# Performance work log

Hardware: AMD Instinct MI355X
Metric: run time of the kernel (lower is better)

Reference implementation:

```python
import jax, jax.numpy as jnp
import numpy as np

N_NODES = 50000
N_EDGES = 800000
VOCAB = 15000
IN_FEATS = 128
HIDDEN = 32
HEADS = 4
N_GRAPHS = 64
NEG_SLOPE = 0.2


def setup_inputs() -> dict:
    key = jax.random.key(0)
    ks = jax.random.split(key, 16)
    word_ids = jax.random.randint(ks[0], (N_NODES,), 0, VOCAB)
    edge_src = jax.random.randint(ks[1], (N_EDGES,), 0, N_NODES)
    edge_dst = jax.random.randint(ks[2], (N_EDGES,), 0, N_NODES)
    node_graph_id = jnp.sort(jax.random.randint(ks[3], (N_NODES,), 0, N_GRAPHS))
    y_data = jax.random.uniform(ks[4], (N_GRAPHS,))
    word_embeds = jax.random.normal(ks[5], (VOCAB, IN_FEATS)) * 0.02
    W0 = jax.random.normal(ks[6], (IN_FEATS, HEADS * HIDDEN)) * (1.0 / np.sqrt(IN_FEATS))
    al0 = jax.random.normal(ks[7], (HEADS, HIDDEN)) * 0.1
    ar0 = jax.random.normal(ks[8], (HEADS, HIDDEN)) * 0.1
    W1 = jax.random.normal(ks[9], (HEADS * HIDDEN, HEADS * HIDDEN)) * (1.0 / np.sqrt(HEADS * HIDDEN))
    al1 = jax.random.normal(ks[10], (HEADS, HIDDEN)) * 0.1
    ar1 = jax.random.normal(ks[11], (HEADS, HIDDEN)) * 0.1
    out_w = jax.random.normal(ks[12], (HEADS * HIDDEN, 1)) * (1.0 / np.sqrt(HEADS * HIDDEN))
    out_b = jnp.zeros((1,))
    return {"word_ids": word_ids, "edge_src": edge_src, "edge_dst": edge_dst,
            "node_graph_id": node_graph_id, "y_data": y_data,
            "word_embeds": word_embeds, "W0": W0, "al0": al0, "ar0": ar0,
            "W1": W1, "al1": al1, "ar1": ar1, "out_w": out_w, "out_b": out_b}


def gat_layer(h, src, dst, W, al, ar):
    # h: [N, Fin] -> feat: [N, H, D]
    feat = (h @ W).reshape(N_NODES, HEADS, HIDDEN)
    el = (feat * al[None]).sum(-1)  # [N, H]
    er = (feat * ar[None]).sum(-1)  # [N, H]
    e = jax.nn.leaky_relu(el[src] + er[dst], NEG_SLOPE)  # [E, H]
    # segment softmax over incoming edges of each dst node
    m = jax.ops.segment_max(e, dst, num_segments=N_NODES)
    m = jnp.where(jnp.isfinite(m), m, 0.0)
    ex = jnp.exp(e - m[dst])
    denom = jax.ops.segment_sum(ex, dst, num_segments=N_NODES)
    alpha = ex / (denom[dst] + 1e-10)  # [E, H]
    msg = feat[src] * alpha[:, :, None]  # [E, H, D]
    out = jax.ops.segment_sum(msg, dst, num_segments=N_NODES)  # [N, H, D]
    return jax.nn.elu(out).reshape(N_NODES, HEADS * HIDDEN)


def reference(word_ids, edge_src, edge_dst, node_graph_id, y_data,
              word_embeds, W0, al0, ar0, W1, al1, ar1, out_w, out_b):
    h = word_embeds[word_ids]  # [N, IN_FEATS]
    h = gat_layer(h, edge_src, edge_dst, W0, al0, ar0)
    h = gat_layer(h, edge_src, edge_dst, W1, al1, ar1)
    # per-graph max pooling over nodes
    pooled = jax.ops.segment_max(h, node_graph_id, num_segments=N_GRAPHS)
    pooled = jnp.where(jnp.isfinite(pooled), pooled, 0.0)  # guard empty graphs
    logits = (pooled @ out_w + out_b).reshape(-1)  # [G]
    # BCE with logits (stable)
    loss = jnp.mean(jnp.maximum(logits, 0.0) - logits * y_data
                    + jnp.log1p(jnp.exp(-jnp.abs(logits))))
    y_pred = jax.nn.sigmoid(logits)[:, None]
    return (loss, y_pred)
```

## Files before the change

kernel.cpp:

```cpp
#include <hip/hip_runtime.h>
#include <math.h>

#define N_NODES 50000
#define N_EDGES 800000
#define HEADS 4
#define N_GRAPHS 64
#define NEG_SLOPE 0.2f
#define LOG2E 1.4426950408889634f
#define SCAN_NB 196
#define POOL_CHUNK 200
#define POOL_NB 250
#define FEAT_NB 782
#define EDGE_Q 200000
#define EDGE_NB 782

typedef __attribute__((ext_vector_type(8))) short bf16x8;
typedef __attribute__((ext_vector_type(4))) float f32x4;

__device__ __forceinline__ unsigned fkey(float f) {
    unsigned u = __float_as_uint(f);
    return (u & 0x80000000u) ? ~u : (u | 0x80000000u);
}
__device__ __forceinline__ float kval(unsigned k) {
    unsigned u = (k & 0x80000000u) ? (k & 0x7FFFFFFFu) : ~k;
    return __uint_as_float(u);
}

__device__ __forceinline__ unsigned short f2bf(float f) {
    unsigned u = __float_as_uint(f);
    u += 0x7FFFu + ((u >> 16) & 1u);
    return (unsigned short)(u >> 16);
}
__device__ __forceinline__ unsigned pack_bf2(float a, float b) {
    return (unsigned)f2bf(a) | ((unsigned)f2bf(b) << 16);
}


__global__ void hist_kernel(const int* __restrict__ dst, int* __restrict__ deg,
                            int* __restrict__ rank) {
    int i = blockIdx.x * 256 + threadIdx.x;
    if (i >= EDGE_Q) return;
    int e0 = i, e1 = i + EDGE_Q, e2 = i + 2 * EDGE_Q, e3 = i + 3 * EDGE_Q;
    int d0 = dst[e0], d1 = dst[e1], d2 = dst[e2], d3 = dst[e3];
    int r0 = atomicAdd(&deg[d0], 1);
    int r1 = atomicAdd(&deg[d1], 1);
    int r2 = atomicAdd(&deg[d2], 1);
    int r3 = atomicAdd(&deg[d3], 1);
    rank[e0] = r0; rank[e1] = r1; rank[e2] = r2; rank[e3] = r3;
}

__global__ void partial_kernel(const int* __restrict__ deg, int* __restrict__ partial) {
    int t = threadIdx.x, b = blockIdx.x;
    int i = b * 256 + t;
    int v = (i < N_NODES) ? deg[i] : 0;
    #pragma unroll
    for (int off = 1; off < 64; off <<= 1) v += __shfl_xor(v, off, 64);
    __shared__ int wsum[4];
    if ((t & 63) == 0) wsum[t >> 6] = v;
    __syncthreads();
    if (t == 0) partial[b] = wsum[0] + wsum[1] + wsum[2] + wsum[3];
}

__global__ void csr_offsets_kernel(const int* __restrict__ deg, const int* __restrict__ partial,
                                   int* __restrict__ row_start) {
    __shared__ int sb[SCAN_NB];
    __shared__ int wsumA[4];
    __shared__ int wsumB[4];
    int t = threadIdx.x, b = blockIdx.x;
    int lane = t & 63, w = t >> 6;
    {
        int v = (t < SCAN_NB) ? partial[t] : 0;
        int incl = v;
        #pragma unroll
        for (int off = 1; off < 64; off <<= 1) {
            int u = __shfl_up(incl, off, 64);
            if (lane >= off) incl += u;
        }
        if (lane == 63) wsumA[w] = incl;
        __syncthreads();
        int woff = 0;
        #pragma unroll
        for (int k = 0; k < 4; ++k) if (k < w) woff += wsumA[k];
        if (t < SCAN_NB) sb[t] = woff + incl - v;
        __syncthreads();
    }
    int i = b * 256 + t;
    int v = (i < N_NODES) ? deg[i] : 0;
    int incl = v;
    #pragma unroll
    for (int off = 1; off < 64; off <<= 1) {
        int u = __shfl_up(incl, off, 64);
        if (lane >= off) incl += u;
    }
    if (lane == 63) wsumB[w] = incl;
    __syncthreads();
    int woff = sb[b];
    #pragma unroll
    for (int k = 0; k < 4; ++k) if (k < w) woff += wsumB[k];
    int excl = woff + incl - v;
    if (i < N_NODES) row_start[i] = excl;
    else if (i == N_NODES) row_start[i] = excl;
}

__device__ __forceinline__ void scatter_body(int bid, const int* __restrict__ src,
                                             const int* __restrict__ dst,
                                             const int* __restrict__ rank,
                                             const int* __restrict__ row_start,
                                             int* __restrict__ csr_src) {
    int i = bid * 256 + threadIdx.x;
    if (i >= EDGE_Q) return;
    int e0 = i, e1 = i + EDGE_Q, e2 = i + 2 * EDGE_Q, e3 = i + 3 * EDGE_Q;
    int d0 = dst[e0], d1 = dst[e1], d2 = dst[e2], d3 = dst[e3];
    int k0 = rank[e0], k1 = rank[e1], k2 = rank[e2], k3 = rank[e3];
    int s0 = src[e0], s1 = src[e1], s2 = src[e2], s3 = src[e3];
    csr_src[row_start[d0] + k0] = s0;
    csr_src[row_start[d1] + k1] = s1;
    csr_src[row_start[d2] + k2] = s2;
    csr_src[row_start[d3] + k3] = s3;
}


__device__ __forceinline__ void wfrag_body(const float* __restrict__ W,
                                           unsigned* __restrict__ wf, int slot) {
    int f = slot >> 6, l = slot & 63;
    int n = l & 15, q = l >> 4;
    int ct = f >> 2, kq = f & 3;
    int col = 16 * ct + n;
    int k0 = 32 * kq + 8 * q;
    uint4 o;
    o.x = pack_bf2(W[(k0 + 0) * 128 + col], W[(k0 + 1) * 128 + col]);
    o.y = pack_bf2(W[(k0 + 2) * 128 + col], W[(k0 + 3) * 128 + col]);
    o.z = pack_bf2(W[(k0 + 4) * 128 + col], W[(k0 + 5) * 128 + col]);
    o.w = pack_bf2(W[(k0 + 6) * 128 + col], W[(k0 + 7) * 128 + col]);
    ((uint4*)wf)[slot] = o;
}

__global__ void prep_kernel(const float* __restrict__ W0, const float* __restrict__ W1,
                            unsigned* __restrict__ wf0, unsigned* __restrict__ wf1,
                            int* __restrict__ deg, unsigned* __restrict__ pkeys) {
    int b = blockIdx.x, t = threadIdx.x;
    if (b < 8) {
        wfrag_body(W0, wf0, b * 256 + t);
    } else if (b < 16) {
        wfrag_body(W1, wf1, (b - 8) * 256 + t);
    } else if (b < 16 + SCAN_NB) {
        int i = (b - 16) * 256 + t;
        if (i < N_NODES) deg[i] = 0;
    } else {
        int i = (b - 16 - SCAN_NB) * 256 + t;
        if (i < N_GRAPHS * 128) pkeys[i] = 0;
    }
}

template<int IN_BF16>
__device__ __forceinline__ void feat_body(int bid, const void* __restrict__ hin,
                                          const int* __restrict__ wid,
                                          const unsigned* __restrict__ wf,
                                          const float* __restrict__ al,
                                          const float* __restrict__ ar,
                                          unsigned* __restrict__ featb,
                                          float* __restrict__ el, float* __restrict__ er) {
    __shared__ unsigned hl[64 * 68];
    int t = threadIdx.x;
    int n0 = bid * 64;
    if (IN_BF16) {
        const uint4* hb4 = (const uint4*)hin;
        #pragma unroll
        for (int r = 0; r < 4; ++r) {
            int i = t + 256 * r;
            int n = i >> 4, q = i & 15;
            uint4 v = {0u, 0u, 0u, 0u};
            int gn = n0 + n;
            if (gn < N_NODES) v = hb4[(size_t)gn * 16 + q];
            *(uint4*)&hl[n * 68 + q * 4] = v;
        }
    } else {
        const float4* h4 = (const float4*)hin;
        #pragma unroll
        for (int r = 0; r < 8; ++r) {
            int i = t + 256 * r;
            int n = i >> 5, q4 = i & 31;
            float4 v = {0.f, 0.f, 0.f, 0.f};
            int gn = n0 + n;
            if (gn < N_NODES) {
                int row = wid ? wid[gn] : gn;
                v = h4[(size_t)row * 32 + q4];
            }
            hl[n * 68 + q4 * 2]     = pack_bf2(v.x, v.y);
            hl[n * 68 + q4 * 2 + 1] = pack_bf2(v.z, v.w);
        }
    }
    __syncthreads();
    int w = t >> 6, lane = t & 63;
    int col = lane & 15, quad = lane >> 4;
    int nbase = n0 + 16 * w;
    bf16x8 afr[4];
    #pragma unroll
    for (int kq = 0; kq < 4; ++kq)
        afr[kq] = *(const bf16x8*)&hl[(16 * w + col) * 68 + 16 * kq + 4 * quad];
    f32x4 acc[8];
    #pragma unroll
    for (int ct = 0; ct < 8; ++ct) acc[ct] = (f32x4){0.f, 0.f, 0.f, 0.f};
    const uint4* wf4 = (const uint4*)wf;
    #pragma unroll
    for (int ct = 0; ct < 8; ++ct) {
        #pragma unroll
        for (int kq = 0; kq < 4; ++kq) {
            uint4 braw = wf4[(ct * 4 + kq) * 64 + lane];
            bf16x8 bfr = *(const bf16x8*)&braw;
            acc[ct] = __builtin_amdgcn_mfma_f32_16x16x32_bf16(afr[kq], bfr, acc[ct], 0, 0, 0);
        }
    }
    #pragma unroll
    for (int ct = 0; ct < 8; ++ct) {
        #pragma unroll
        for (int reg = 0; reg < 4; ++reg) {
            float v = acc[ct][reg];
            float pv = __shfl_xor(v, 1, 64);
            int node = nbase + quad * 4 + reg;
            if (!(col & 1) && node < N_NODES)
                featb[(size_t)node * 64 + ct * 8 + (col >> 1)] = pack_bf2(v, pv);
        }
    }
    float alv[8], arv[8];
    #pragma unroll
    for (int ct = 0; ct < 8; ++ct) {
        alv[ct] = al[ct * 16 + col];
        arv[ct] = ar[ct * 16 + col];
    }
    #pragma unroll
    for (int reg = 0; reg < 4; ++reg) {
        int node = nbase + quad * 4 + reg;
        #pragma unroll
        for (int hd = 0; hd < 4; ++hd) {
            float pl = acc[2 * hd][reg] * alv[2 * hd] + acc[2 * hd + 1][reg] * alv[2 * hd + 1];
            float pr = acc[2 * hd][reg] * arv[2 * hd] + acc[2 * hd + 1][reg] * arv[2 * hd + 1];
            #pragma unroll
            for (int off = 1; off < 16; off <<= 1) {
                pl += __shfl_xor(pl, off, 64);
                pr += __shfl_xor(pr, off, 64);
            }
            if (col == hd && node < N_NODES) {
                el[node * 4 + hd] = pl * LOG2E;
                er[node * 4 + hd] = pr * LOG2E;
            }
        }
    }
}

template<int IN_BF16>
__global__ __launch_bounds__(256)
void feat_kernel_t(const void* __restrict__ hin, const int* __restrict__ wid,
                   const unsigned* __restrict__ wf,
                   const float* __restrict__ al, const float* __restrict__ ar,
                   unsigned* __restrict__ featb, float* __restrict__ el,
                   float* __restrict__ er) {
    feat_body<IN_BF16>(blockIdx.x, hin, wid, wf, al, ar, featb, el, er);
}

__global__ __launch_bounds__(256)
void scatter_feat0_kernel(const int* __restrict__ src, const int* __restrict__ dst,
                          const int* __restrict__ rank, const int* __restrict__ row_start,
                          int* __restrict__ csr_src,
                          const float* __restrict__ emb, const int* __restrict__ wid,
                          const unsigned* __restrict__ wf0,
                          const float* __restrict__ al0, const float* __restrict__ ar0,
                          unsigned* __restrict__ featb, float* __restrict__ el,
                          float* __restrict__ er) {
    if (blockIdx.x < EDGE_NB) {
        scatter_body(blockIdx.x, src, dst, rank, row_start, csr_src);
    } else {
        feat_body<0>(blockIdx.x - EDGE_NB, emb, wid, wf0, al0, ar0, featb, el, er);
    }
}

template<int OUT_BF16>
__global__ void gat_aggregate_t(const int* __restrict__ row_start, const int* __restrict__ csr_src,
                                const unsigned* __restrict__ featb, const float* __restrict__ el,
                                const float* __restrict__ er, float* __restrict__ houtf,
                                unsigned* __restrict__ houtb) {
    int lane = threadIdx.x & 63;
    int d = blockIdx.x * 4 + (threadIdx.x >> 6);
    int beg = row_start[d], end = row_start[d + 1];
    int eg = lane >> 4;
    int li = lane & 15;
    int hc = li >> 2;
    float er_h = er[d * 4 + hc];
    float a0 = 0.f, a1 = 0.f, a2 = 0.f, a3 = 0.f;
    float a4 = 0.f, a5 = 0.f, a6 = 0.f, a7 = 0.f;
    float dsum = 0.f;
    int b8 = beg + ((end - beg) & ~7);
    for (int base = beg; base < b8; base += 8) {
        int ea = base + eg, eb = base + 4 + eg;
        int sa = csr_src[ea];
        int sb = csr_src[eb];
        float la = el[sa * 4 + hc];
        float lb = el[sb * 4 + hc];
        uint4 pa = *(const uint4*)(featb + (size_t)sa * 64 + li * 4);
        uint4 pb = *(const uint4*)(featb + (size_t)sb * 64 + li * 4);
        float va = la + er_h; va = fmaxf(va, NEG_SLOPE * va);
        float vb = lb + er_h; vb = fmaxf(vb, NEG_SLOPE * vb);
        float xa = exp2f(va), xb = exp2f(vb);
        dsum += xa + xb;
        a0 += __uint_as_float(pa.x << 16) * xa;
        a1 += __uint_as_float(pa.x & 0xFFFF0000u) * xa;
        a2 += __uint_as_float(pa.y << 16) * xa;
        a3 += __uint_as_float(pa.y & 0xFFFF0000u) * xa;
        a4 += __uint_as_float(pa.z << 16) * xa;
        a5 += __uint_as_float(pa.z & 0xFFFF0000u) * xa;
        a6 += __uint_as_float(pa.w << 16) * xa;
        a7 += __uint_as_float(pa.w & 0xFFFF0000u) * xa;
        a0 += __uint_as_float(pb.x << 16) * xb;
        a1 += __uint_as_float(pb.x & 0xFFFF0000u) * xb;
        a2 += __uint_as_float(pb.y << 16) * xb;
        a3 += __uint_as_float(pb.y & 0xFFFF0000u) * xb;
        a4 += __uint_as_float(pb.z << 16) * xb;
        a5 += __uint_as_float(pb.z & 0xFFFF0000u) * xb;
        a6 += __uint_as_float(pb.w << 16) * xb;
        a7 += __uint_as_float(pb.w & 0xFFFF0000u) * xb;
    }
    for (int ee = b8 + eg; ee < end; ee += 4) {
        int s = csr_src[ee];
        float lv = el[s * 4 + hc];
        uint4 pv = *(const uint4*)(featb + (size_t)s * 64 + li * 4);
        float v = lv + er_h; v = fmaxf(v, NEG_SLOPE * v);
        float x = exp2f(v);
        dsum += x;
        a0 += __uint_as_float(pv.x << 16) * x;
        a1 += __uint_as_float(pv.x & 0xFFFF0000u) * x;
        a2 += __uint_as_float(pv.y << 16) * x;
        a3 += __uint_as_float(pv.y & 0xFFFF0000u) * x;
        a4 += __uint_as_float(pv.z << 16) * x;
        a5 += __uint_as_float(pv.z & 0xFFFF0000u) * x;
        a6 += __uint_as_float(pv.w << 16) * x;
        a7 += __uint_as_float(pv.w & 0xFFFF0000u) * x;
    }
    #pragma unroll
    for (int off = 16; off < 64; off <<= 1) {
        a0 += __shfl_xor(a0, off, 64);
        a1 += __shfl_xor(a1, off, 64);
        a2 += __shfl_xor(a2, off, 64);
        a3 += __shfl_xor(a3, off, 64);
        a4 += __shfl_xor(a4, off, 64);
        a5 += __shfl_xor(a5, off, 64);
        a6 += __shfl_xor(a6, off, 64);
        a7 += __shfl_xor(a7, off, 64);
        dsum += __shfl_xor(dsum, off, 64);
    }
    if (eg == 0) {
        float inv = 1.f / (dsum + 1e-10f);
        float o0 = a0 * inv, o1 = a1 * inv, o2 = a2 * inv, o3 = a3 * inv;
        float o4 = a4 * inv, o5 = a5 * inv, o6 = a6 * inv, o7 = a7 * inv;
        o0 = o0 > 0.f ? o0 : expm1f(o0);
        o1 = o1 > 0.f ? o1 : expm1f(o1);
        o2 = o2 > 0.f ? o2 : expm1f(o2);
        o3 = o3 > 0.f ? o3 : expm1f(o3);
        o4 = o4 > 0.f ? o4 : expm1f(o4);
        o5 = o5 > 0.f ? o5 : expm1f(o5);
        o6 = o6 > 0.f ? o6 : expm1f(o6);
        o7 = o7 > 0.f ? o7 : expm1f(o7);
        if (OUT_BF16) {
            uint4 wv;
            wv.x = pack_bf2(o0, o1);
            wv.y = pack_bf2(o2, o3);
            wv.z = pack_bf2(o4, o5);
            wv.w = pack_bf2(o6, o7);
            ((uint4*)(houtb + (size_t)d * 64))[li] = wv;
        } else {
            float4* op = (float4*)(houtf + (size_t)d * 128);
            float4 w0 = {o0, o1, o2, o3};
            float4 w1 = {o4, o5, o6, o7};
            op[li * 2] = w0;
            op[li * 2 + 1] = w1;
        }
    }
}


__global__ void pool_kernel(const int* __restrict__ gid, const float* __restrict__ h,
                            unsigned* __restrict__ pkeys) {
    int t = threadIdx.x;
    int c = t & 127;
    int par = t >> 7;
    int n0 = blockIdx.x * POOL_CHUNK;
    float m = 0.f;
    int cur_g = -1;
    for (int n = n0 + par; n < n0 + POOL_CHUNK; n += 2) {
        int g = gid[n];
        if (g != cur_g) {
            if (cur_g >= 0) atomicMax(&pkeys[cur_g * 128 + c], fkey(m));
            cur_g = g;
            m = -3.0e38f;
        }
        m = fmaxf(m, h[(size_t)n * 128 + c]);
    }
    if (cur_g >= 0) atomicMax(&pkeys[cur_g * 128 + c], fkey(m));
}

__global__ void logits_final_kernel(const unsigned* __restrict__ pkeys,
                                    const float* __restrict__ w, const float* __restrict__ bptr,
                                    const float* __restrict__ y, float* __restrict__ out) {
    __shared__ float slog[N_GRAPHS];
    int t = threadIdx.x;
    int wv = t >> 6, lane = t & 63;
    float b = bptr[0];
    #pragma unroll
    for (int k = 0; k < 16; ++k) {
        int g = wv * 16 + k;
        float sum = 0.f;
        #pragma unroll
        for (int c0 = 0; c0 < 128; c0 += 64) {
            int c = c0 + lane;
            unsigned kk = pkeys[g * 128 + c];
            float v = (kk == 0u) ? 0.f : kval(kk);
            sum += v * w[c];
        }
        #pragma unroll
        for (int off = 32; off; off >>= 1) sum += __shfl_down(sum, off, 64);
        if (lane == 0) slog[g] = sum + b;
    }
    __syncthreads();
    if (t < N_GRAPHS) {
        float l = slog[t];
        float term = fmaxf(l, 0.f) - l * y[t] + log1pf(expf(-fabsf(l)));
        float s = term;
        #pragma unroll
        for (int off = 32; off; off >>= 1) s += __shfl_down(s, off, 64);
        out[1 + t] = 1.f / (1.f + expf(-l));
        if (t == 0) out[0] = s * (1.f / 64.f);
    }
}

extern "C" void kernel_launch(void* const* d_in, const int* in_sizes, int n_in,
                              void* d_out, int out_size, void* d_ws, size_t ws_size,
                              hipStream_t stream) {
    const int* word_ids  = (const int*)d_in[0];
    const int* esrc      = (const int*)d_in[1];
    const int* edst      = (const int*)d_in[2];
    const int* gid       = (const int*)d_in[3];
    const float* y_data  = (const float*)d_in[4];
    const float* emb     = (const float*)d_in[5];
    const float* W0      = (const float*)d_in[6];
    const float* al0     = (const float*)d_in[7];
    const float* ar0     = (const float*)d_in[8];
    const float* W1      = (const float*)d_in[9];
    const float* al1     = (const float*)d_in[10];
    const float* ar1     = (const float*)d_in[11];
    const float* out_w   = (const float*)d_in[12];
    const float* out_b   = (const float*)d_in[13];
    float* out = (float*)d_out;

    float* ws = (float*)d_ws;
    unsigned* featb  = (unsigned*)ws;
    unsigned* hb     = (unsigned*)(ws + 3200000);
    float*    hout   = ws + 6400000;
    float*    el     = ws + 12800000;
    float*    er     = ws + 13000000;
    int*      row_st = (int*)(ws + 13200000);
    int*      deg    = (int*)(ws + 13250004);
    int*      rank   = (int*)(ws + 13300004);
    int*      csrsrc = (int*)(ws + 14100004);
    int*      partial= (int*)(ws + 14900004);
    unsigned* pkeys  = (unsigned*)(ws + 14900204);
    unsigned* wf0    = (unsigned*)(ws + 14908396);
    unsigned* wf1    = (unsigned*)(ws + 14916588);

    prep_kernel<<<16 + SCAN_NB + 32, 256, 0, stream>>>(W0, W1, wf0, wf1, deg, pkeys);
    hist_kernel<<<EDGE_NB, 256, 0, stream>>>(edst, deg, rank);
    partial_kernel<<<SCAN_NB, 256, 0, stream>>>(deg, partial);
    csr_offsets_kernel<<<SCAN_NB, 256, 0, stream>>>(deg, partial, row_st);

    scatter_feat0_kernel<<<EDGE_NB + FEAT_NB, 256, 0, stream>>>(
        esrc, edst, rank, row_st, csrsrc, emb, word_ids, wf0, al0, ar0, featb, el, er);

    gat_aggregate_t<1><<<12500, 256, 0, stream>>>(row_st, csrsrc, featb, el, er, nullptr, hb);
    feat_kernel_t<1><<<FEAT_NB, 256, 0, stream>>>(hb, nullptr, wf1, al1, ar1, featb, el, er);
    gat_aggregate_t<0><<<12500, 256, 0, stream>>>(row_st, csrsrc, featb, el, er, hout, nullptr);

    pool_kernel<<<POOL_NB, 256, 0, stream>>>(gid, hout, pkeys);
    logits_final_kernel<<<1, 256, 0, stream>>>(pkeys, out_w, out_b, y_data, out);
}
```

Measured before the change: 297.9 us.

## Split aggregation per head with head-major feature layout for cache locality

Stores bf16 node features in head-major planes (one 64-byte row per node per head) and launches the aggregation kernel four times as many blocks, each block handling one head for four destination nodes. Each wave now gathers 16 edges at a time with 4 lanes per edge over a single head plane, so concurrently running blocks touch a smaller feature working set. The aim is better L2 reuse of gathered rows. The cost is that CSR indices, el values and row bounds are re-read once per head. Pool chunking is also retuned to more, smaller blocks.

```diff
diff --git a/kernel.cpp b/kernel.cpp
--- a/kernel.cpp
+++ b/kernel.cpp
@@ -8,9 +8,10 @@
 #define NEG_SLOPE 0.2f
 #define LOG2E 1.4426950408889634f
 #define SCAN_NB 196
-#define POOL_CHUNK 200
-#define POOL_NB 250
+#define POOL_CHUNK 50
+#define POOL_NB 1000
 #define FEAT_NB 782
+#define AGG_NB 12500
 #define EDGE_Q 200000
 #define EDGE_NB 782
 
@@ -168,11 +169,12 @@
         #pragma unroll
         for (int r = 0; r < 4; ++r) {
             int i = t + 256 * r;
-            int n = i >> 4, q = i & 15;
+            int n = i >> 4, qq = i & 15;
             uint4 v = {0u, 0u, 0u, 0u};
             int gn = n0 + n;
-            if (gn < N_NODES) v = hb4[(size_t)gn * 16 + q];
-            *(uint4*)&hl[n * 68 + q * 4] = v;
+            if (gn < N_NODES)
+                v = hb4[((size_t)(qq >> 2) * N_NODES + gn) * 4 + (qq & 3)];
+            *(uint4*)&hl[n * 68 + qq * 4] = v;
         }
     } else {
         const float4* h4 = (const float4*)hin;
@@ -219,7 +221,8 @@
             float pv = __shfl_xor(v, 1, 64);
             int node = nbase + quad * 4 + reg;
             if (!(col & 1) && node < N_NODES)
-                featb[(size_t)node * 64 + ct * 8 + (col >> 1)] = pack_bf2(v, pv);
+                featb[((size_t)(ct >> 1) * N_NODES + node) * 16 + (ct & 1) * 8 + (col >> 1)]
+                    = pack_bf2(v, pv);
         }
     }
     float alv[8], arv[8];
@@ -275,54 +278,28 @@
 }
 
 template<int OUT_BF16>
-__global__ void gat_aggregate_t(const int* __restrict__ row_start, const int* __restrict__ csr_src,
+__global__ void gat_aggregate_q(const int* __restrict__ row_start, const int* __restrict__ csr_src,
                                 const unsigned* __restrict__ featb, const float* __restrict__ el,
                                 const float* __restrict__ er, float* __restrict__ houtf,
                                 unsigned* __restrict__ houtb) {
+    int bid = blockIdx.x;
+    int q = bid / AGG_NB;
+    int db = bid - q * AGG_NB;
     int lane = threadIdx.x & 63;
-    int d = blockIdx.x * 4 + (threadIdx.x >> 6);
+    int d = db * 4 + (threadIdx.x >> 6);
     int beg = row_start[d], end = row_start[d + 1];
-    int eg = lane >> 4;
-    int li = lane & 15;
-    int hc = li >> 2;
-    float er_h = er[d * 4 + hc];
+    int eg = lane >> 2;
+    int li = lane & 3;
+    float er_h = er[d * 4 + q];
+    const unsigned* fq = featb + (size_t)q * N_NODES * 16;
     float a0 = 0.f, a1 = 0.f, a2 = 0.f, a3 = 0.f;
     float a4 = 0.f, a5 = 0.f, a6 = 0.f, a7 = 0.f;
     float dsum = 0.f;
-    int b8 = beg + ((end - beg) & ~7);
-    for (int base = beg; base < b8; base += 8) {
-        int ea = base + eg, eb = base + 4 + eg;
-        int sa = csr_src[ea];
-        int sb = csr_src[eb];
-        float la = el[sa * 4 + hc];
-        float lb = el[sb * 4 + hc];
-        uint4 pa = *(const uint4*)(featb + (size_t)sa * 64 + li * 4);
-        uint4 pb = *(const uint4*)(featb + (size_t)sb * 64 + li * 4);
-        float va = la + er_h; va = fmaxf(va, NEG_SLOPE * va);
-        float vb = lb + er_h; vb = fmaxf(vb, NEG_SLOPE * vb);
-        float xa = exp2f(va), xb = exp2f(vb);
-        dsum += xa + xb;
-        a0 += __uint_as_float(pa.x << 16) * xa;
-        a1 += __uint_as_float(pa.x & 0xFFFF0000u) * xa;
-        a2 += __uint_as_float(pa.y << 16) * xa;
-        a3 += __uint_as_float(pa.y & 0xFFFF0000u) * xa;
-        a4 += __uint_as_float(pa.z << 16) * xa;
-        a5 += __uint_as_float(pa.z & 0xFFFF0000u) * xa;
-        a6 += __uint_as_float(pa.w << 16) * xa;
-        a7 += __uint_as_float(pa.w & 0xFFFF0000u) * xa;
-        a0 += __uint_as_float(pb.x << 16) * xb;
-        a1 += __uint_as_float(pb.x & 0xFFFF0000u) * xb;
-        a2 += __uint_as_float(pb.y << 16) * xb;
-        a3 += __uint_as_float(pb.y & 0xFFFF0000u) * xb;
-        a4 += __uint_as_float(pb.z << 16) * xb;
-        a5 += __uint_as_float(pb.z & 0xFFFF0000u) * xb;
-        a6 += __uint_as_float(pb.w << 16) * xb;
-        a7 += __uint_as_float(pb.w & 0xFFFF0000u) * xb;
-    }
-    for (int ee = b8 + eg; ee < end; ee += 4) {
-        int s = csr_src[ee];
-        float lv = el[s * 4 + hc];
-        uint4 pv = *(const uint4*)(featb + (size_t)s * 64 + li * 4);
+    int b16 = beg + ((end - beg) & ~15);
+    for (int base = beg; base < b16; base += 16) {
+        int s = csr_src[base + eg];
+        float lv = el[s * 4 + q];
+        uint4 pv = *(const uint4*)(fq + (size_t)s * 16 + li * 4);
         float v = lv + er_h; v = fmaxf(v, NEG_SLOPE * v);
         float x = exp2f(v);
         dsum += x;
@@ -335,8 +312,24 @@
         a6 += __uint_as_float(pv.w << 16) * x;
         a7 += __uint_as_float(pv.w & 0xFFFF0000u) * x;
     }
-    #pragma unroll
-    for (int off = 16; off < 64; off <<= 1) {
+    for (int ee = b16 + eg; ee < end; ee += 16) {
+        int s = csr_src[ee];
+        float lv = el[s * 4 + q];
+        uint4 pv = *(const uint4*)(fq + (size_t)s * 16 + li * 4);
+        float v = lv + er_h; v = fmaxf(v, NEG_SLOPE * v);
+        float x = exp2f(v);
+        dsum += x;
+        a0 += __uint_as_float(pv.x << 16) * x;
+        a1 += __uint_as_float(pv.x & 0xFFFF0000u) * x;
+        a2 += __uint_as_float(pv.y << 16) * x;
+        a3 += __uint_as_float(pv.y & 0xFFFF0000u) * x;
+        a4 += __uint_as_float(pv.z << 16) * x;
+        a5 += __uint_as_float(pv.z & 0xFFFF0000u) * x;
+        a6 += __uint_as_float(pv.w << 16) * x;
+        a7 += __uint_as_float(pv.w & 0xFFFF0000u) * x;
+    }
+    #pragma unroll
+    for (int off = 4; off < 64; off <<= 1) {
         a0 += __shfl_xor(a0, off, 64);
         a1 += __shfl_xor(a1, off, 64);
         a2 += __shfl_xor(a2, off, 64);
@@ -365,13 +358,13 @@
             wv.y = pack_bf2(o2, o3);
             wv.z = pack_bf2(o4, o5);
             wv.w = pack_bf2(o6, o7);
-            ((uint4*)(houtb + (size_t)d * 64))[li] = wv;
+            ((uint4*)(houtb + ((size_t)q * N_NODES + d) * 16))[li] = wv;
         } else {
-            float4* op = (float4*)(houtf + (size_t)d * 128);
+            float4* op = (float4*)(houtf + (size_t)d * 128 + q * 32 + li * 8);
             float4 w0 = {o0, o1, o2, o3};
             float4 w1 = {o4, o5, o6, o7};
-            op[li * 2] = w0;
-            op[li * 2 + 1] = w1;
+            op[0] = w0;
+            op[1] = w1;
         }
     }
 }
@@ -473,9 +466,9 @@
     scatter_feat0_kernel<<<EDGE_NB + FEAT_NB, 256, 0, stream>>>(
         esrc, edst, rank, row_st, csrsrc, emb, word_ids, wf0, al0, ar0, featb, el, er);
 
-    gat_aggregate_t<1><<<12500, 256, 0, stream>>>(row_st, csrsrc, featb, el, er, nullptr, hb);
+    gat_aggregate_q<1><<<4 * AGG_NB, 256, 0, stream>>>(row_st, csrsrc, featb, el, er, nullptr, hb);
     feat_kernel_t<1><<<FEAT_NB, 256, 0, stream>>>(hb, nullptr, wf1, al1, ar1, featb, el, er);
-    gat_aggregate_t<0><<<12500, 256, 0, stream>>>(row_st, csrsrc, featb, el, er, hout, nullptr);
+    gat_aggregate_q<0><<<4 * AGG_NB, 256, 0, stream>>>(row_st, csrsrc, featb, el, er, hout, nullptr);
 
     pool_kernel<<<POOL_NB, 256, 0, stream>>>(gid, hout, pkeys);
     logits_final_kernel<<<1, 256, 0, stream>>>(pkeys, out_w, out_b, y_data, out);
```

Result: slower. 384.4 us (+29.0%).

## Replace stored edge ranks with atomic cursor scatter, fast ELU, finer pool chunks

Applied to the files above, without the earlier changes.

The histogram pass no longer records a per-edge rank. The scatter pass now claims CSR slots with atomicAdd on a per-node cursor initialised from row_start, which removes the 3.2MB rank write and reread and the row_start gather, at the cost of a second round of atomics. ELU now uses exp2f instead of expm1f, and pooling is split into more, smaller chunks for more parallelism. Neighbor order inside each CSR row becomes nondeterministic, so float summation order can vary from run to run.

```diff
diff --git a/kernel.cpp b/kernel.cpp
--- a/kernel.cpp
+++ b/kernel.cpp
@@ -8,8 +8,8 @@
 #define NEG_SLOPE 0.2f
 #define LOG2E 1.4426950408889634f
 #define SCAN_NB 196
-#define POOL_CHUNK 200
-#define POOL_NB 250
+#define POOL_CHUNK 50
+#define POOL_NB 1000
 #define FEAT_NB 782
 #define EDGE_Q 200000
 #define EDGE_NB 782
@@ -35,18 +35,20 @@
     return (unsigned)f2bf(a) | ((unsigned)f2bf(b) << 16);
 }
 
-
-__global__ void hist_kernel(const int* __restrict__ dst, int* __restrict__ deg,
-                            int* __restrict__ rank) {
+__device__ __forceinline__ float elu_fast(float o) {
+    float e = exp2f(o * LOG2E) - 1.f;
+    return o > 0.f ? o : e;
+}
+
+
+__global__ void hist_kernel(const int* __restrict__ dst, int* __restrict__ deg) {
     int i = blockIdx.x * 256 + threadIdx.x;
     if (i >= EDGE_Q) return;
-    int e0 = i, e1 = i + EDGE_Q, e2 = i + 2 * EDGE_Q, e3 = i + 3 * EDGE_Q;
-    int d0 = dst[e0], d1 = dst[e1], d2 = dst[e2], d3 = dst[e3];
-    int r0 = atomicAdd(&deg[d0], 1);
-    int r1 = atomicAdd(&deg[d1], 1);
-    int r2 = atomicAdd(&deg[d2], 1);
-    int r3 = atomicAdd(&deg[d3], 1);
-    rank[e0] = r0; rank[e1] = r1; rank[e2] = r2; rank[e3] = r3;
+    int d0 = dst[i], d1 = dst[i + EDGE_Q], d2 = dst[i + 2 * EDGE_Q], d3 = dst[i + 3 * EDGE_Q];
+    atomicAdd(&deg[d0], 1);
+    atomicAdd(&deg[d1], 1);
+    atomicAdd(&deg[d2], 1);
+    atomicAdd(&deg[d3], 1);
 }
 
 __global__ void partial_kernel(const int* __restrict__ deg, int* __restrict__ partial) {
@@ -62,7 +64,7 @@
 }
 
 __global__ void csr_offsets_kernel(const int* __restrict__ deg, const int* __restrict__ partial,
-                                   int* __restrict__ row_start) {
+                                   int* __restrict__ row_start, int* __restrict__ cursor) {
     __shared__ int sb[SCAN_NB];
     __shared__ int wsumA[4];
     __shared__ int wsumB[4];
@@ -98,25 +100,27 @@
     #pragma unroll
     for (int k = 0; k < 4; ++k) if (k < w) woff += wsumB[k];
     int excl = woff + incl - v;
-    if (i < N_NODES) row_start[i] = excl;
+    if (i < N_NODES) { row_start[i] = excl; cursor[i] = excl; }
     else if (i == N_NODES) row_start[i] = excl;
 }
 
 __device__ __forceinline__ void scatter_body(int bid, const int* __restrict__ src,
                                              const int* __restrict__ dst,
-                                             const int* __restrict__ rank,
-                                             const int* __restrict__ row_start,
+                                             int* __restrict__ cursor,
                                              int* __restrict__ csr_src) {
     int i = bid * 256 + threadIdx.x;
     if (i >= EDGE_Q) return;
     int e0 = i, e1 = i + EDGE_Q, e2 = i + 2 * EDGE_Q, e3 = i + 3 * EDGE_Q;
     int d0 = dst[e0], d1 = dst[e1], d2 = dst[e2], d3 = dst[e3];
-    int k0 = rank[e0], k1 = rank[e1], k2 = rank[e2], k3 = rank[e3];
     int s0 = src[e0], s1 = src[e1], s2 = src[e2], s3 = src[e3];
-    csr_src[row_start[d0] + k0] = s0;
-    csr_src[row_start[d1] + k1] = s1;
-    csr_src[row_start[d2] + k2] = s2;
-    csr_src[row_start[d3] + k3] = s3;
+    int p0 = atomicAdd(&cursor[d0], 1);
+    int p1 = atomicAdd(&cursor[d1], 1);
+    int p2 = atomicAdd(&cursor[d2], 1);
+    int p3 = atomicAdd(&cursor[d3], 1);
+    csr_src[p0] = s0;
+    csr_src[p1] = s1;
+    csr_src[p2] = s2;
+    csr_src[p3] = s3;
 }
 
 
@@ -260,15 +264,14 @@
 
 __global__ __launch_bounds__(256)
 void scatter_feat0_kernel(const int* __restrict__ src, const int* __restrict__ dst,
-                          const int* __restrict__ rank, const int* __restrict__ row_start,
-                          int* __restrict__ csr_src,
+                          int* __restrict__ cursor, int* __restrict__ csr_src,
                           const float* __restrict__ emb, const int* __restrict__ wid,
                           const unsigned* __restrict__ wf0,
                           const float* __restrict__ al0, const float* __restrict__ ar0,
                           unsigned* __restrict__ featb, float* __restrict__ el,
                           float* __restrict__ er) {
     if (blockIdx.x < EDGE_NB) {
-        scatter_body(blockIdx.x, src, dst, rank, row_start, csr_src);
+        scatter_body(blockIdx.x, src, dst, cursor, csr_src);
     } else {
         feat_body<0>(blockIdx.x - EDGE_NB, emb, wid, wf0, al0, ar0, featb, el, er);
     }
@@ -349,16 +352,10 @@
     }
     if (eg == 0) {
         float inv = 1.f / (dsum + 1e-10f);
-        float o0 = a0 * inv, o1 = a1 * inv, o2 = a2 * inv, o3 = a3 * inv;
-        float o4 = a4 * inv, o5 = a5 * inv, o6 = a6 * inv, o7 = a7 * inv;
-        o0 = o0 > 0.f ? o0 : expm1f(o0);
-        o1 = o1 > 0.f ? o1 : expm1f(o1);
-        o2 = o2 > 0.f ? o2 : expm1f(o2);
-        o3 = o3 > 0.f ? o3 : expm1f(o3);
-        o4 = o4 > 0.f ? o4 : expm1f(o4);
-        o5 = o5 > 0.f ? o5 : expm1f(o5);
-        o6 = o6 > 0.f ? o6 : expm1f(o6);
-        o7 = o7 > 0.f ? o7 : expm1f(o7);
+        float o0 = elu_fast(a0 * inv), o1 = elu_fast(a1 * inv);
+        float o2 = elu_fast(a2 * inv), o3 = elu_fast(a3 * inv);
+        float o4 = elu_fast(a4 * inv), o5 = elu_fast(a5 * inv);
+        float o6 = elu_fast(a6 * inv), o7 = elu_fast(a7 * inv);
         if (OUT_BF16) {
             uint4 wv;
             wv.x = pack_bf2(o0, o1);
@@ -458,20 +455,20 @@
     float*    er     = ws + 13000000;
     int*      row_st = (int*)(ws + 13200000);
     int*      deg    = (int*)(ws + 13250004);
-    int*      rank   = (int*)(ws + 13300004);
-    int*      csrsrc = (int*)(ws + 14100004);
-    int*      partial= (int*)(ws + 14900004);
-    unsigned* pkeys  = (unsigned*)(ws + 14900204);
-    unsigned* wf0    = (unsigned*)(ws + 14908396);
-    unsigned* wf1    = (unsigned*)(ws + 14916588);
+    int*      cursor = (int*)(ws + 13300004);
+    int*      csrsrc = (int*)(ws + 13350008);
+    int*      partial= (int*)(ws + 14150008);
+    unsigned* pkeys  = (unsigned*)(ws + 14150208);
+    unsigned* wf0    = (unsigned*)(ws + 14158400);
+    unsigned* wf1    = (unsigned*)(ws + 14166592);
 
     prep_kernel<<<16 + SCAN_NB + 32, 256, 0, stream>>>(W0, W1, wf0, wf1, deg, pkeys);
-    hist_kernel<<<EDGE_NB, 256, 0, stream>>>(edst, deg, rank);
+    hist_kernel<<<EDGE_NB, 256, 0, stream>>>(edst, deg);
     partial_kernel<<<SCAN_NB, 256, 0, stream>>>(deg, partial);
-    csr_offsets_kernel<<<SCAN_NB, 256, 0, stream>>>(deg, partial, row_st);
+    csr_offsets_kernel<<<SCAN_NB, 256, 0, stream>>>(deg, partial, row_st, cursor);
 
     scatter_feat0_kernel<<<EDGE_NB + FEAT_NB, 256, 0, stream>>>(
-        esrc, edst, rank, row_st, csrsrc, emb, word_ids, wf0, al0, ar0, featb, el, er);
+        esrc, edst, cursor, csrsrc, emb, word_ids, wf0, al0, ar0, featb, el, er);
 
     gat_aggregate_t<1><<<12500, 256, 0, stream>>>(row_st, csrsrc, featb, el, er, nullptr, hb);
     feat_kernel_t<1><<<FEAT_NB, 256, 0, stream>>>(hb, nullptr, wf1, al1, ar1, featb, el, er);
```

New measurement: 311.3 us. 4.5% more time.
